# Performance work log

Measured on AMD Instinct MI355X. Metric: run time of the kernel, lower is better.

## Reference

```python
import jax, jax.numpy as jnp
import numpy as np

QUANT_BLOCK = 32  # GGUF Q4_0-style block size
QUANT_ZERO = 8.0  # 4-bit codes are offset-binary around 8


def setup_inputs() -> dict:
    key = jax.random.key(0)
    k_x, k_q, k_s, k_up, k_dn, k_b = jax.random.split(key, 6)
    O, I, R = 4096, 4096, 16
    T = 2048  # tokens (batch*seq)
    x = jax.random.normal(k_x, (T, I), dtype=jnp.float32)
    # quantized 4-bit codes stored unpacked as int32 in [0, 16)
    q = jax.random.randint(k_q, (O, I), 0, 16, dtype=jnp.int32)
    # per-block scales (small positive, like real GGUF d values)
    scales = jax.random.uniform(k_s, (O, I // QUANT_BLOCK), dtype=jnp.float32) * 0.05
    lora_up = jax.random.normal(k_up, (O, R), dtype=jnp.float32) * 0.02
    lora_down = jax.random.normal(k_dn, (R, I), dtype=jnp.float32) * 0.02
    alpha = jnp.ones((), dtype=jnp.float32)
    bias = jax.random.normal(k_b, (O,), dtype=jnp.float32)
    return {"x": x, "q": q, "scales": scales, "lora_up": lora_up,
            "lora_down": lora_down, "alpha": alpha, "bias": bias}


def _dequant(q, scales):
    # q: [O, I] int codes; scales: [O, I/BLOCK] per-block scale
    O, I = q.shape
    qf = q.reshape(O, I // QUANT_BLOCK, QUANT_BLOCK).astype(scales.dtype)
    w = (qf - QUANT_ZERO) * scales[:, :, None]  # [O, I/B, B]
    return w.reshape(O, I)


def reference(x, q, scales, lora_up, lora_down, alpha, bias):
    # on-the-fly dequant (GGMLLayer.get_weight -> dequantize_tensor)
    W = _dequant(q, scales)  # [O, I]
    # LoRA patch apply (ray_calculate_weight): W += alpha * up @ down
    W = W + alpha * jnp.einsum('or,ri->oi', lora_up, lora_down)
    # linear forward: y = x @ W^T + b
    return jnp.einsum('ti,oi->to', x, W) + bias
```

## Files before the change

kernel.cpp:

```cpp
#include <hip/hip_runtime.h>
#include <hip/hip_bf16.h>
#include <stdint.h>

#define T_DIM 2048
#define I_DIM 4096
#define O_DIM 4096
#define R_DIM 16
#define QBLK  32

typedef __bf16 bf16x8 __attribute__((ext_vector_type(8)));
typedef float  floatx4 __attribute__((ext_vector_type(4)));
typedef unsigned short ushort_t;

#define AS1 __attribute__((address_space(1)))
#define AS3 __attribute__((address_space(3)))

__device__ __forceinline__ ushort_t f2bf(float f) {
  unsigned u = __float_as_uint(f);
  u += 0x7FFFu + ((u >> 16) & 1u);
  return (ushort_t)(u >> 16);
}

__device__ __forceinline__ float dot4(float4 a, float4 b) {
  return a.x * b.x + a.y * b.y + a.z * b.z + a.w * b.w;
}

__global__ __launch_bounds__(256) void k_stream(const float* __restrict__ x,
                                                const int* __restrict__ q,
                                                const float* __restrict__ scales,
                                                ushort_t* __restrict__ xb,
                                                ushort_t* __restrict__ wb) {
  const int b = blockIdx.x, tid = threadIdx.x;
  if (b < 4096) {
    int idx = b * 256 + tid;
    const float4* xp = (const float4*)x;
    float4 a = xp[idx * 2], c = xp[idx * 2 + 1];
    union { ushort_t u[8]; uint4 v; } r;
    r.u[0] = f2bf(a.x); r.u[1] = f2bf(a.y); r.u[2] = f2bf(a.z); r.u[3] = f2bf(a.w);
    r.u[4] = f2bf(c.x); r.u[5] = f2bf(c.y); r.u[6] = f2bf(c.z); r.u[7] = f2bf(c.w);
    ((uint4*)xb)[idx] = r.v;
    return;
  }
  {
    int idx = (b - 4096) * 256 + tid;
    int o  = idx >> 9;
    int i0 = (idx & 511) * 8;
    float s = scales[o * (I_DIM / QBLK) + (i0 >> 5)];
    const int4* qp = (const int4*)(q + (size_t)o * I_DIM + i0);
    int4 q0 = qp[0], q1 = qp[1];
    union { ushort_t u[8]; uint4 v; } r;
    r.u[0] = f2bf((float)(q0.x - 8) * s); r.u[1] = f2bf((float)(q0.y - 8) * s);
    r.u[2] = f2bf((float)(q0.z - 8) * s); r.u[3] = f2bf((float)(q0.w - 8) * s);
    r.u[4] = f2bf((float)(q1.x - 8) * s); r.u[5] = f2bf((float)(q1.y - 8) * s);
    r.u[6] = f2bf((float)(q1.z - 8) * s); r.u[7] = f2bf((float)(q1.w - 8) * s);
    ((uint4*)wb)[idx] = r.v;
  }
}

__global__ __launch_bounds__(256) void k_xd(const float* __restrict__ x,
                                            const float* __restrict__ down,
                                            const float* __restrict__ alphap,
                                            float* __restrict__ xd) {
  __shared__ float ds[16 * 512];
  const int b = blockIdx.x, tid = threadIdx.x;
  const int tl = tid >> 5, s = tid & 31;
  const int t = b * 8 + tl;
  float acc[16];
#pragma unroll
  for (int r = 0; r < 16; ++r) acc[r] = 0.f;
  for (int c = 0; c < 8; ++c) {
    const int ib = c * 512;
    __syncthreads();
#pragma unroll
    for (int j = 0; j < 8; ++j) {
      int e = j * 256 + tid;
      int r = e >> 7, col = e & 127;
      ((float4*)ds)[e] = ((const float4*)(down + (size_t)r * I_DIM + ib))[col];
    }
    __syncthreads();
#pragma unroll
    for (int j = 0; j < 4; ++j) {
      float4 xv = ((const float4*)(x + (size_t)t * I_DIM + ib))[s + 32 * j];
#pragma unroll
      for (int r = 0; r < 16; ++r) {
        float4 dv = ((const float4*)ds)[r * 128 + s + 32 * j];
        acc[r] += dot4(xv, dv);
      }
    }
  }
  const float al = alphap[0];
#pragma unroll
  for (int r = 0; r < 16; ++r) {
    float v = acc[r];
    v += __shfl_down(v, 16, 32);
    v += __shfl_down(v, 8, 32);
    v += __shfl_down(v, 4, 32);
    v += __shfl_down(v, 2, 32);
    v += __shfl_down(v, 1, 32);
    if (s == 0) xd[t * 16 + r] = v * al;
  }
}


#define BK 64
#define NT (I_DIM / BK)
#define ASZ (128 * BK)
#define BSZ (256 * BK)

__device__ __forceinline__ bf16x8 lds_read16(unsigned addr) {
  bf16x8 d;
  asm volatile("ds_read_b128 %0, %1" : "=v"(d) : "v"(addr));
  return d;
}

__device__ __forceinline__ void stage6(const ushort_t* __restrict__ ga,
                                       const ushort_t* __restrict__ gb,
                                       ushort_t* Ast, ushort_t* Bst, int tid) {
#pragma unroll
  for (int it = 0; it < 2; ++it) {
    const int seg = it * 512 + tid;
    const int r = seg >> 3, cg = (seg & 7) ^ (r & 7);
    __builtin_amdgcn_global_load_lds(
        (const AS1 char*)(ga + (size_t)r * I_DIM + cg * 8),
        (AS3 char*)(Ast + (size_t)seg * 8), 16, 0, 0);
  }
#pragma unroll
  for (int it = 0; it < 4; ++it) {
    const int seg = it * 512 + tid;
    const int r = seg >> 3, cg = (seg & 7) ^ (r & 7);
    __builtin_amdgcn_global_load_lds(
        (const AS1 char*)(gb + (size_t)r * I_DIM + cg * 8),
        (AS3 char*)(Bst + (size_t)seg * 8), 16, 0, 0);
  }
}

template<int VM, bool STG>
__device__ __forceinline__ void ktile(unsigned aB, unsigned bB,
                                      ushort_t* Ast, ushort_t* Bst,
                                      const ushort_t* ga, const ushort_t* gb,
                                      floatx4 (&acc)[4][4], int tid) {
  const int lane = tid & 63, wv = tid >> 6;
  const int quad = lane >> 4, m16 = lane & 15;
  const int wm = wv >> 2, wn = wv & 3;

  if constexpr (STG) stage6(ga, gb, Ast, Bst, tid);

  bf16x8 a0[4], b0[4], a1[4], b1[4];
#pragma unroll
  for (int i = 0; i < 4; ++i) {
    const int m = wm * 64 + i * 16 + m16;
    a0[i] = lds_read16(aB + (unsigned)((m * 8 + (quad ^ (m & 7))) * 16));
  }
#pragma unroll
  for (int i = 0; i < 4; ++i) {
    const int n = wn * 64 + i * 16 + m16;
    b0[i] = lds_read16(bB + (unsigned)((n * 8 + (quad ^ (n & 7))) * 16));
  }
#pragma unroll
  for (int i = 0; i < 4; ++i) {
    const int m = wm * 64 + i * 16 + m16;
    a1[i] = lds_read16(aB + (unsigned)((m * 8 + ((4 + quad) ^ (m & 7))) * 16));
  }
#pragma unroll
  for (int i = 0; i < 4; ++i) {
    const int n = wn * 64 + i * 16 + m16;
    b1[i] = lds_read16(bB + (unsigned)((n * 8 + ((4 + quad) ^ (n & 7))) * 16));
  }
  asm volatile("s_waitcnt lgkmcnt(8)" ::: "memory");
  __builtin_amdgcn_sched_barrier(0);
  __builtin_amdgcn_s_setprio(1);
#pragma unroll
  for (int i = 0; i < 4; ++i)
#pragma unroll
    for (int j = 0; j < 4; ++j)
      acc[i][j] = __builtin_amdgcn_mfma_f32_16x16x32_bf16(a0[i], b0[j], acc[i][j], 0, 0, 0);
  __builtin_amdgcn_s_setprio(0);
  asm volatile("s_waitcnt lgkmcnt(0)" ::: "memory");
  __builtin_amdgcn_sched_barrier(0);
  __builtin_amdgcn_s_setprio(1);
#pragma unroll
  for (int i = 0; i < 4; ++i)
#pragma unroll
    for (int j = 0; j < 4; ++j)
      acc[i][j] = __builtin_amdgcn_mfma_f32_16x16x32_bf16(a1[i], b1[j], acc[i][j], 0, 0, 0);
  __builtin_amdgcn_s_setprio(0);
  if constexpr (VM == 6)      asm volatile("s_waitcnt vmcnt(6)" ::: "memory");
  else if constexpr (VM == 0) asm volatile("s_waitcnt vmcnt(0)" ::: "memory");
  if constexpr (VM >= 0) __builtin_amdgcn_sched_barrier(0);
  __builtin_amdgcn_s_barrier();
}

__global__ __launch_bounds__(512, 2) void k_gemm(const ushort_t* __restrict__ xb,
                                                 const ushort_t* __restrict__ wb,
                                                 const float* __restrict__ bias,
                                                 const float* __restrict__ xd,
                                                 const float* __restrict__ up,
                                                 float* __restrict__ y) {
  __shared__ __align__(16) ushort_t As[3][ASZ];
  __shared__ __align__(16) ushort_t Bs[3][BSZ];

  const int tid = threadIdx.x;
  const int oT = blockIdx.x * 256, tT = blockIdx.y * 128;
  const ushort_t* ap = xb + (size_t)tT * I_DIM;
  const ushort_t* bp = wb + (size_t)oT * I_DIM;

  const unsigned aL = (unsigned)(uintptr_t)(AS3 ushort_t*)&As[0][0];
  const unsigned bL = (unsigned)(uintptr_t)(AS3 ushort_t*)&Bs[0][0];
  const unsigned aS0 = aL, aS1 = aL + ASZ * 2, aS2 = aL + ASZ * 4;
  const unsigned bS0 = bL, bS1 = bL + BSZ * 2, bS2 = bL + BSZ * 4;

  floatx4 acc[4][4] = {};

  stage6(ap, bp, As[0], Bs[0], tid);
  stage6(ap + BK, bp + BK, As[1], Bs[1], tid);
  asm volatile("s_waitcnt vmcnt(6)" ::: "memory");
  __builtin_amdgcn_sched_barrier(0);
  __builtin_amdgcn_s_barrier();

  int kc = 2 * BK;
  for (int g = 0; g < 20; ++g) {
    ktile<6, true>(aS0, bS0, As[2], Bs[2], ap + kc, bp + kc, acc, tid); kc += BK;
    ktile<6, true>(aS1, bS1, As[0], Bs[0], ap + kc, bp + kc, acc, tid); kc += BK;
    ktile<6, true>(aS2, bS2, As[1], Bs[1], ap + kc, bp + kc, acc, tid); kc += BK;
  }
  ktile<6, true>(aS0, bS0, As[2], Bs[2], ap + kc, bp + kc, acc, tid); kc += BK;
  ktile<6, true>(aS1, bS1, As[0], Bs[0], ap + kc, bp + kc, acc, tid);
  ktile<0, false>(aS2, bS2, nullptr, nullptr, nullptr, nullptr, acc, tid);
  ktile<-1, false>(aS0, bS0, nullptr, nullptr, nullptr, nullptr, acc, tid);

  const int lane = tid & 63, wv = tid >> 6;
  const int quad = lane >> 4, m16 = lane & 15;
  const int wm = wv >> 2, wn = wv & 3;
#pragma unroll
  for (int im = 0; im < 4; ++im) {
#pragma unroll
    for (int reg = 0; reg < 4; ++reg) {
      const int t = tT + wm * 64 + im * 16 + quad * 4 + reg;
      const float4* xr = (const float4*)(xd + t * 16);
      float4 x0 = xr[0], x1 = xr[1], x2 = xr[2], x3 = xr[3];
#pragma unroll
      for (int in_ = 0; in_ < 4; ++in_) {
        const int o = oT + wn * 64 + in_ * 16 + m16;
        const float4* ur = (const float4*)(up + (size_t)o * R_DIM);
        float lv = dot4(x0, ur[0]) + dot4(x1, ur[1]) +
                   dot4(x2, ur[2]) + dot4(x3, ur[3]);
        y[(size_t)t * O_DIM + o] = acc[im][in_][reg] + lv + bias[o];
      }
    }
  }
}

extern "C" void kernel_launch(void* const* d_in, const int* in_sizes, int n_in,
                              void* d_out, int out_size, void* d_ws, size_t ws_size,
                              hipStream_t stream) {
  const float* x      = (const float*)d_in[0];
  const int*   q      = (const int*)d_in[1];
  const float* scales = (const float*)d_in[2];
  const float* up     = (const float*)d_in[3];
  const float* down   = (const float*)d_in[4];
  const float* alpha  = (const float*)d_in[5];
  const float* bias   = (const float*)d_in[6];
  float* y = (float*)d_out;

  ushort_t* xb = (ushort_t*)d_ws;
  ushort_t* wb = (ushort_t*)((char*)d_ws + (size_t)T_DIM * I_DIM * 2);
  float*    xd = (float*)((char*)d_ws + (size_t)T_DIM * I_DIM * 2 + (size_t)O_DIM * I_DIM * 2);

  hipLaunchKernelGGL(k_stream, dim3(4096 + 8192), dim3(256), 0, stream,
                     x, q, scales, xb, wb);
  hipLaunchKernelGGL(k_xd, dim3(256), dim3(256), 0, stream, x, down, alpha, xd);
  hipLaunchKernelGGL(k_gemm, dim3(O_DIM / 256, T_DIM / 128), dim3(512), 0, stream,
                     xb, wb, bias, xd, up, y);
}
```

Baseline: 435.3 us.

## Fuse x conversion and Q4 dequant into GEMM main loop via register staging

Removes the separate streaming kernel that converted x to bf16 and dequantized q into a bf16 weight buffer. The GEMM now loads fp32 x and int32 codes plus scales straight into registers, converts and dequantizes them, and writes swizzled bf16 tiles to LDS. This avoids the round trip of the intermediate buffers through memory and one kernel launch. In exchange, each block re-reads wider fp32/int32 data on every k-step, the pipeline drops from triple-buffered async global-to-LDS loads to register-staged double buffering, and launch bounds drop to one block per CU.

```diff
diff --git a/kernel.cpp b/kernel.cpp
--- a/kernel.cpp
+++ b/kernel.cpp
@@ -15,46 +15,10 @@
 #define AS1 __attribute__((address_space(1)))
 #define AS3 __attribute__((address_space(3)))
 
-__device__ __forceinline__ ushort_t f2bf(float f) {
-  unsigned u = __float_as_uint(f);
-  u += 0x7FFFu + ((u >> 16) & 1u);
-  return (ushort_t)(u >> 16);
-}
+typedef bf16x8 AS3* bf16x8_lds;
 
 __device__ __forceinline__ float dot4(float4 a, float4 b) {
   return a.x * b.x + a.y * b.y + a.z * b.z + a.w * b.w;
-}
-
-__global__ __launch_bounds__(256) void k_stream(const float* __restrict__ x,
-                                                const int* __restrict__ q,
-                                                const float* __restrict__ scales,
-                                                ushort_t* __restrict__ xb,
-                                                ushort_t* __restrict__ wb) {
-  const int b = blockIdx.x, tid = threadIdx.x;
-  if (b < 4096) {
-    int idx = b * 256 + tid;
-    const float4* xp = (const float4*)x;
-    float4 a = xp[idx * 2], c = xp[idx * 2 + 1];
-    union { ushort_t u[8]; uint4 v; } r;
-    r.u[0] = f2bf(a.x); r.u[1] = f2bf(a.y); r.u[2] = f2bf(a.z); r.u[3] = f2bf(a.w);
-    r.u[4] = f2bf(c.x); r.u[5] = f2bf(c.y); r.u[6] = f2bf(c.z); r.u[7] = f2bf(c.w);
-    ((uint4*)xb)[idx] = r.v;
-    return;
-  }
-  {
-    int idx = (b - 4096) * 256 + tid;
-    int o  = idx >> 9;
-    int i0 = (idx & 511) * 8;
-    float s = scales[o * (I_DIM / QBLK) + (i0 >> 5)];
-    const int4* qp = (const int4*)(q + (size_t)o * I_DIM + i0);
-    int4 q0 = qp[0], q1 = qp[1];
-    union { ushort_t u[8]; uint4 v; } r;
-    r.u[0] = f2bf((float)(q0.x - 8) * s); r.u[1] = f2bf((float)(q0.y - 8) * s);
-    r.u[2] = f2bf((float)(q0.z - 8) * s); r.u[3] = f2bf((float)(q0.w - 8) * s);
-    r.u[4] = f2bf((float)(q1.x - 8) * s); r.u[5] = f2bf((float)(q1.y - 8) * s);
-    r.u[6] = f2bf((float)(q1.z - 8) * s); r.u[7] = f2bf((float)(q1.w - 8) * s);
-    ((uint4*)wb)[idx] = r.v;
-  }
 }
 
 __global__ __launch_bounds__(256) void k_xd(const float* __restrict__ x,
@@ -104,8 +68,8 @@
 
 #define BK 64
 #define NT (I_DIM / BK)
-#define ASZ (128 * BK)
-#define BSZ (256 * BK)
+#define A_ELEMS (128 * BK)
+#define B_ELEMS (256 * BK)
 
 __device__ __forceinline__ bf16x8 lds_read16(unsigned addr) {
   bf16x8 d;
@@ -113,124 +77,152 @@
   return d;
 }
 
-__device__ __forceinline__ void stage6(const ushort_t* __restrict__ ga,
-                                       const ushort_t* __restrict__ gb,
-                                       ushort_t* Ast, ushort_t* Bst, int tid) {
+struct StageRegs {
+  float4 ax[2][2];
+  int4   qv[4][2];
+  float  sc[4];
+};
+
+__device__ __forceinline__ void gload(StageRegs& R,
+                                      const float* __restrict__ x,
+                                      const int* __restrict__ q,
+                                      const float* __restrict__ scales,
+                                      int k0, int tT, int oT, int tid) {
 #pragma unroll
   for (int it = 0; it < 2; ++it) {
-    const int seg = it * 512 + tid;
-    const int r = seg >> 3, cg = (seg & 7) ^ (r & 7);
-    __builtin_amdgcn_global_load_lds(
-        (const AS1 char*)(ga + (size_t)r * I_DIM + cg * 8),
-        (AS3 char*)(Ast + (size_t)seg * 8), 16, 0, 0);
+    const int e = it * 512 + tid, r = e >> 3, c8 = e & 7;
+    const float4* p = (const float4*)(x + (size_t)(tT + r) * I_DIM + k0 + c8 * 8);
+    R.ax[it][0] = p[0]; R.ax[it][1] = p[1];
   }
 #pragma unroll
   for (int it = 0; it < 4; ++it) {
-    const int seg = it * 512 + tid;
-    const int r = seg >> 3, cg = (seg & 7) ^ (r & 7);
-    __builtin_amdgcn_global_load_lds(
-        (const AS1 char*)(gb + (size_t)r * I_DIM + cg * 8),
-        (AS3 char*)(Bst + (size_t)seg * 8), 16, 0, 0);
-  }
-}
-
-template<int VM, bool STG>
-__device__ __forceinline__ void ktile(unsigned aB, unsigned bB,
-                                      ushort_t* Ast, ushort_t* Bst,
-                                      const ushort_t* ga, const ushort_t* gb,
-                                      floatx4 (&acc)[4][4], int tid) {
+    const int e = it * 512 + tid, r = e >> 3, c8 = e & 7;
+    const int4* p = (const int4*)(q + (size_t)(oT + r) * I_DIM + k0 + c8 * 8);
+    R.qv[it][0] = p[0]; R.qv[it][1] = p[1];
+    R.sc[it] = scales[(size_t)(oT + r) * (I_DIM / QBLK) + ((k0 + c8 * 8) >> 5)];
+  }
+}
+
+__device__ __forceinline__ void dswrite(const StageRegs& R,
+                                        AS3 ushort_t* A0, AS3 ushort_t* B0,
+                                        int tid) {
+#pragma unroll
+  for (int it = 0; it < 2; ++it) {
+    const int e = it * 512 + tid, r = e >> 3, c8 = e & 7, g = c8 ^ (r & 7);
+    const float4 lo = R.ax[it][0], hi = R.ax[it][1];
+    bf16x8 v;
+    v[0] = (__bf16)lo.x; v[1] = (__bf16)lo.y; v[2] = (__bf16)lo.z; v[3] = (__bf16)lo.w;
+    v[4] = (__bf16)hi.x; v[5] = (__bf16)hi.y; v[6] = (__bf16)hi.z; v[7] = (__bf16)hi.w;
+    *(bf16x8_lds)(A0 + (size_t)(r * 8 + g) * 8) = v;
+  }
+#pragma unroll
+  for (int it = 0; it < 4; ++it) {
+    const int e = it * 512 + tid, r = e >> 3, c8 = e & 7, g = c8 ^ (r & 7);
+    const float s = R.sc[it], n8 = -8.0f * s;
+    const int4 q0 = R.qv[it][0], q1 = R.qv[it][1];
+    bf16x8 v;
+    v[0] = (__bf16)fmaf((float)q0.x, s, n8);
+    v[1] = (__bf16)fmaf((float)q0.y, s, n8);
+    v[2] = (__bf16)fmaf((float)q0.z, s, n8);
+    v[3] = (__bf16)fmaf((float)q0.w, s, n8);
+    v[4] = (__bf16)fmaf((float)q1.x, s, n8);
+    v[5] = (__bf16)fmaf((float)q1.y, s, n8);
+    v[6] = (__bf16)fmaf((float)q1.z, s, n8);
+    v[7] = (__bf16)fmaf((float)q1.w, s, n8);
+    *(bf16x8_lds)(B0 + (size_t)(r * 8 + g) * 8) = v;
+  }
+}
+
+__global__ __launch_bounds__(512, 1) void k_fused(const float* __restrict__ x,
+                                                  const int* __restrict__ q,
+                                                  const float* __restrict__ scales,
+                                                  const float* __restrict__ bias,
+                                                  const float* __restrict__ xd,
+                                                  const float* __restrict__ up,
+                                                  float* __restrict__ y) {
+  __shared__ __align__(16) ushort_t Ab[2][A_ELEMS];
+  __shared__ __align__(16) ushort_t Bb[2][B_ELEMS];
+
+  const int tid = threadIdx.x;
   const int lane = tid & 63, wv = tid >> 6;
   const int quad = lane >> 4, m16 = lane & 15;
   const int wm = wv >> 2, wn = wv & 3;
 
-  if constexpr (STG) stage6(ga, gb, Ast, Bst, tid);
-
-  bf16x8 a0[4], b0[4], a1[4], b1[4];
-#pragma unroll
-  for (int i = 0; i < 4; ++i) {
-    const int m = wm * 64 + i * 16 + m16;
-    a0[i] = lds_read16(aB + (unsigned)((m * 8 + (quad ^ (m & 7))) * 16));
-  }
-#pragma unroll
-  for (int i = 0; i < 4; ++i) {
-    const int n = wn * 64 + i * 16 + m16;
-    b0[i] = lds_read16(bB + (unsigned)((n * 8 + (quad ^ (n & 7))) * 16));
-  }
-#pragma unroll
-  for (int i = 0; i < 4; ++i) {
-    const int m = wm * 64 + i * 16 + m16;
-    a1[i] = lds_read16(aB + (unsigned)((m * 8 + ((4 + quad) ^ (m & 7))) * 16));
-  }
-#pragma unroll
-  for (int i = 0; i < 4; ++i) {
-    const int n = wn * 64 + i * 16 + m16;
-    b1[i] = lds_read16(bB + (unsigned)((n * 8 + ((4 + quad) ^ (n & 7))) * 16));
-  }
-  asm volatile("s_waitcnt lgkmcnt(8)" ::: "memory");
+  const int oT = blockIdx.x * 256, tT = blockIdx.y * 128;
+
+  const unsigned aL = (unsigned)(uintptr_t)(AS3 ushort_t*)&Ab[0][0];
+  const unsigned bL = (unsigned)(uintptr_t)(AS3 ushort_t*)&Bb[0][0];
+
+  floatx4 acc[4][4] = {};
+  StageRegs R;
+
+  gload(R, x, q, scales, 0, tT, oT, tid);
+  asm volatile("s_waitcnt vmcnt(0)" ::: "memory");
   __builtin_amdgcn_sched_barrier(0);
-  __builtin_amdgcn_s_setprio(1);
-#pragma unroll
-  for (int i = 0; i < 4; ++i)
-#pragma unroll
-    for (int j = 0; j < 4; ++j)
-      acc[i][j] = __builtin_amdgcn_mfma_f32_16x16x32_bf16(a0[i], b0[j], acc[i][j], 0, 0, 0);
-  __builtin_amdgcn_s_setprio(0);
+  dswrite(R, (AS3 ushort_t*)&Ab[0][0], (AS3 ushort_t*)&Bb[0][0], tid);
+  gload(R, x, q, scales, BK, tT, oT, tid);
   asm volatile("s_waitcnt lgkmcnt(0)" ::: "memory");
   __builtin_amdgcn_sched_barrier(0);
-  __builtin_amdgcn_s_setprio(1);
-#pragma unroll
-  for (int i = 0; i < 4; ++i)
-#pragma unroll
-    for (int j = 0; j < 4; ++j)
-      acc[i][j] = __builtin_amdgcn_mfma_f32_16x16x32_bf16(a1[i], b1[j], acc[i][j], 0, 0, 0);
-  __builtin_amdgcn_s_setprio(0);
-  if constexpr (VM == 6)      asm volatile("s_waitcnt vmcnt(6)" ::: "memory");
-  else if constexpr (VM == 0) asm volatile("s_waitcnt vmcnt(0)" ::: "memory");
-  if constexpr (VM >= 0) __builtin_amdgcn_sched_barrier(0);
   __builtin_amdgcn_s_barrier();
-}
-
-__global__ __launch_bounds__(512, 2) void k_gemm(const ushort_t* __restrict__ xb,
-                                                 const ushort_t* __restrict__ wb,
-                                                 const float* __restrict__ bias,
-                                                 const float* __restrict__ xd,
-                                                 const float* __restrict__ up,
-                                                 float* __restrict__ y) {
-  __shared__ __align__(16) ushort_t As[3][ASZ];
-  __shared__ __align__(16) ushort_t Bs[3][BSZ];
-
-  const int tid = threadIdx.x;
-  const int oT = blockIdx.x * 256, tT = blockIdx.y * 128;
-  const ushort_t* ap = xb + (size_t)tT * I_DIM;
-  const ushort_t* bp = wb + (size_t)oT * I_DIM;
-
-  const unsigned aL = (unsigned)(uintptr_t)(AS3 ushort_t*)&As[0][0];
-  const unsigned bL = (unsigned)(uintptr_t)(AS3 ushort_t*)&Bs[0][0];
-  const unsigned aS0 = aL, aS1 = aL + ASZ * 2, aS2 = aL + ASZ * 4;
-  const unsigned bS0 = bL, bS1 = bL + BSZ * 2, bS2 = bL + BSZ * 4;
-
-  floatx4 acc[4][4] = {};
-
-  stage6(ap, bp, As[0], Bs[0], tid);
-  stage6(ap + BK, bp + BK, As[1], Bs[1], tid);
-  asm volatile("s_waitcnt vmcnt(6)" ::: "memory");
-  __builtin_amdgcn_sched_barrier(0);
-  __builtin_amdgcn_s_barrier();
-
-  int kc = 2 * BK;
-  for (int g = 0; g < 20; ++g) {
-    ktile<6, true>(aS0, bS0, As[2], Bs[2], ap + kc, bp + kc, acc, tid); kc += BK;
-    ktile<6, true>(aS1, bS1, As[0], Bs[0], ap + kc, bp + kc, acc, tid); kc += BK;
-    ktile<6, true>(aS2, bS2, As[1], Bs[1], ap + kc, bp + kc, acc, tid); kc += BK;
-  }
-  ktile<6, true>(aS0, bS0, As[2], Bs[2], ap + kc, bp + kc, acc, tid); kc += BK;
-  ktile<6, true>(aS1, bS1, As[0], Bs[0], ap + kc, bp + kc, acc, tid);
-  ktile<0, false>(aS2, bS2, nullptr, nullptr, nullptr, nullptr, acc, tid);
-  ktile<-1, false>(aS0, bS0, nullptr, nullptr, nullptr, nullptr, acc, tid);
-
-  const int lane = tid & 63, wv = tid >> 6;
-  const int quad = lane >> 4, m16 = lane & 15;
-  const int wm = wv >> 2, wn = wv & 3;
+
+  for (int kt = 0; kt < NT; ++kt) {
+    const int cur = kt & 1;
+    const unsigned aB = aL + (unsigned)cur * (A_ELEMS * 2);
+    const unsigned bB = bL + (unsigned)cur * (B_ELEMS * 2);
+
+    bf16x8 a0[4], b0[4], a1[4], b1[4];
+#pragma unroll
+    for (int i = 0; i < 4; ++i) {
+      const int m = wm * 64 + i * 16 + m16;
+      a0[i] = lds_read16(aB + (unsigned)((m * 8 + (quad ^ (m & 7))) * 16));
+    }
+#pragma unroll
+    for (int i = 0; i < 4; ++i) {
+      const int n = wn * 64 + i * 16 + m16;
+      b0[i] = lds_read16(bB + (unsigned)((n * 8 + (quad ^ (n & 7))) * 16));
+    }
+#pragma unroll
+    for (int i = 0; i < 4; ++i) {
+      const int m = wm * 64 + i * 16 + m16;
+      a1[i] = lds_read16(aB + (unsigned)((m * 8 + ((4 + quad) ^ (m & 7))) * 16));
+    }
+#pragma unroll
+    for (int i = 0; i < 4; ++i) {
+      const int n = wn * 64 + i * 16 + m16;
+      b1[i] = lds_read16(bB + (unsigned)((n * 8 + ((4 + quad) ^ (n & 7))) * 16));
+    }
+    asm volatile("s_waitcnt lgkmcnt(8)" ::: "memory");
+    __builtin_amdgcn_sched_barrier(0);
+    __builtin_amdgcn_s_setprio(1);
+#pragma unroll
+    for (int i = 0; i < 4; ++i)
+#pragma unroll
+      for (int j = 0; j < 4; ++j)
+        acc[i][j] = __builtin_amdgcn_mfma_f32_16x16x32_bf16(a0[i], b0[j], acc[i][j], 0, 0, 0);
+    __builtin_amdgcn_s_setprio(0);
+    asm volatile("s_waitcnt lgkmcnt(0)" ::: "memory");
+    __builtin_amdgcn_sched_barrier(0);
+    __builtin_amdgcn_s_setprio(1);
+#pragma unroll
+    for (int i = 0; i < 4; ++i)
+#pragma unroll
+      for (int j = 0; j < 4; ++j)
+        acc[i][j] = __builtin_amdgcn_mfma_f32_16x16x32_bf16(a1[i], b1[j], acc[i][j], 0, 0, 0);
+    __builtin_amdgcn_s_setprio(0);
+
+    if (kt < NT - 1) {
+      asm volatile("s_waitcnt vmcnt(0)" ::: "memory");
+      __builtin_amdgcn_sched_barrier(0);
+      __builtin_amdgcn_s_barrier();
+      dswrite(R, (AS3 ushort_t*)&Ab[cur ^ 1][0], (AS3 ushort_t*)&Bb[cur ^ 1][0], tid);
+      if (kt < NT - 2)
+        gload(R, x, q, scales, (kt + 2) * BK, tT, oT, tid);
+      asm volatile("s_waitcnt lgkmcnt(0)" ::: "memory");
+      __builtin_amdgcn_sched_barrier(0);
+      __builtin_amdgcn_s_barrier();
+    }
+  }
+
 #pragma unroll
   for (int im = 0; im < 4; ++im) {
 #pragma unroll
@@ -262,13 +254,9 @@
   const float* bias   = (const float*)d_in[6];
   float* y = (float*)d_out;
 
-  ushort_t* xb = (ushort_t*)d_ws;
-  ushort_t* wb = (ushort_t*)((char*)d_ws + (size_t)T_DIM * I_DIM * 2);
-  float*    xd = (float*)((char*)d_ws + (size_t)T_DIM * I_DIM * 2 + (size_t)O_DIM * I_DIM * 2);
-
-  hipLaunchKernelGGL(k_stream, dim3(4096 + 8192), dim3(256), 0, stream,
-                     x, q, scales, xb, wb);
+  float* xd = (float*)d_ws;
+
   hipLaunchKernelGGL(k_xd, dim3(256), dim3(256), 0, stream, x, down, alpha, xd);
-  hipLaunchKernelGGL(k_gemm, dim3(O_DIM / 256, T_DIM / 128), dim3(512), 0, stream,
-                     xb, wb, bias, xd, up, y);
-}
+  hipLaunchKernelGGL(k_fused, dim3(O_DIM / 256, T_DIM / 128), dim3(512), 0, stream,
+                     x, q, scales, bias, xd, up, y);
+}
```

New measurement: 503.7 us. 1.16x slower.
